# Kernel optimization log

Measured on AMD Instinct MI355X. Metric: run time of the kernel, lower is better.

Reference implementation:

```python
import jax, jax.numpy as jnp
import numpy as np

BN_EPS = 1e-5


def conv1x1(x, W, b):
    # x: [B, Cin, N], W: [Cout, Cin], b: [Cout]
    return jnp.einsum('oc,bcn->bon', W, x) + b[None, :, None]


def bn(x, p):
    # p: [4, C] rows = gamma, beta, running_mean, running_var (inference BN)
    g, be, m, v = p[0], p[1], p[2], p[3]
    inv = jax.lax.rsqrt(v + BN_EPS)
    return (x - m[None, :, None]) * (g * inv)[None, :, None] + be[None, :, None]


def conv_bn_relu(x, W, b, p):
    return jax.nn.relu(bn(conv1x1(x, W, b), p))


def _make_params(key, cout, cin):
    k1, k2 = jax.random.split(key)
    W = jax.random.normal(k1, (cout, cin), jnp.float32) * (1.0 / np.sqrt(cin))
    b = jax.random.normal(k2, (cout,), jnp.float32) * 0.01
    p = jnp.stack([jnp.ones(cout), jnp.zeros(cout), jnp.zeros(cout), jnp.ones(cout)]).astype(jnp.float32)
    return W, b, p


def setup_inputs() -> dict:
    key = jax.random.key(0)
    ks = jax.random.split(key, 16)
    B, N, S, D1, D2 = 2, 16384, 4096, 128, 256
    Cin, C, Cm = D1 + D2 + 13, 128, 128  # 397, out_channel, mlp[0]
    inp = {
        'xyz1': jax.random.normal(ks[0], (B, N, 3), jnp.float32),
        'xyz2': jax.random.normal(ks[1], (B, S, 3), jnp.float32),
        'points1': jax.random.normal(ks[2], (B, D1, N), jnp.float32),
        'points2': jax.random.normal(ks[3], (B, D2, S), jnp.float32),
        'last_pred': jax.random.normal(ks[4], (B, S, 13), jnp.float32),
    }
    inp['fuse_W'], inp['fuse_b'], inp['fuse_bn'] = _make_params(ks[5], C, Cin)
    inp['ext1_W'], inp['ext1_b'], inp['ext1_bn'] = _make_params(ks[6], C, C)
    inp['ext2_W'], inp['ext2_b'], inp['ext2_bn'] = _make_params(ks[7], C, C)
    inp['pred1_W'], inp['pred1_b'], inp['pred1_bn'] = _make_params(ks[8], Cm, C)
    inp['pred2_W'], inp['pred2_b'], inp['pred2_bn'] = _make_params(ks[9], 13, Cm)
    return inp


def _forward(xyz1, xyz2, points1, points2, last_pred,
             fuse_W, fuse_b, fuse_bn, ext1_W, ext1_b, ext1_bn,
             ext2_W, ext2_b, ext2_bn, pred1_W, pred1_b, pred1_bn,
             pred2_W, pred2_b, pred2_bn):
    B, N, _ = xyz1.shape
    p1 = jnp.transpose(points1, (0, 2, 1))  # [B, N, D1]
    p2 = jnp.transpose(points2, (0, 2, 1))  # [B, S, D2]
    # squared distances [B, N, S]
    dists = (jnp.sum(xyz1 ** 2, -1)[:, :, None]
             + jnp.sum(xyz2 ** 2, -1)[:, None, :]
             - 2.0 * jnp.einsum('bnc,bsc->bns', xyz1, xyz2))
    # 3 smallest distances (partial top-k instead of full sort; same math)
    neg_d3, idx = jax.lax.top_k(-dists, 3)  # [B, N, 3]
    d3 = -neg_d3
    recip = 1.0 / (d3 + 1e-8)
    weight = recip / jnp.sum(recip, axis=2, keepdims=True)  # [B, N, 3]
    bidx = jnp.arange(B)[:, None, None]
    interp_pts = jnp.sum(p2[bidx, idx] * weight[..., None], axis=2)        # [B, N, D2]
    interp_pred = jnp.sum(last_pred[bidx, idx] * weight[..., None], axis=2)  # [B, N, 13]
    new_points = jnp.transpose(jnp.concatenate([p1, interp_pts, interp_pred], axis=-1), (0, 2, 1))  # [B, Cin, N]
    # fuse
    x = conv_bn_relu(new_points, fuse_W, fuse_b, fuse_bn)
    # extraction: one ConvBNReLURes1D block (groups=1, res_expansion=1)
    h = conv_bn_relu(x, ext1_W, ext1_b, ext1_bn)
    x = jax.nn.relu(bn(conv1x1(h, ext2_W, ext2_b), ext2_bn) + x)  # [B, C, N]
    new_points_out = x
    # prediction head (dropout is identity in eval mode)
    feat = conv_bn_relu(x, pred1_W, pred1_b, pred1_bn)
    pred = conv_bn_relu(feat, pred2_W, pred2_b, pred2_bn)
    return (new_points_out,
            jnp.transpose(feat, (0, 2, 1)),
            jnp.transpose(pred, (0, 2, 1)))


def reference(xyz1, xyz2, points1, points2, last_pred,
              fuse_W, fuse_b, fuse_bn, ext1_W, ext1_b, ext1_bn,
              ext2_W, ext2_b, ext2_bn, pred1_W, pred1_b, pred1_bn,
              pred2_W, pred2_b, pred2_bn):
    return _forward(xyz1, xyz2, points1, points2, last_pred,
                    fuse_W, fuse_b, fuse_bn, ext1_W, ext1_b, ext1_bn,
                    ext2_W, ext2_b, ext2_bn, pred1_W, pred1_b, pred1_bn,
                    pred2_W, pred2_b, pred2_bn)
```

## Files before the change

kernel.cpp:

```cpp
#include <hip/hip_runtime.h>
#include <stdint.h>

#define B_   2
#define N_   16384
#define S_   4096
#define D2_  256
#define CIN_ 397
#define KP_  416
#define C_   128
#define OC_  13
#define NCHUNK_ 16
#define CHS_ (S_ / NCHUNK_)
#define NCAND_ (NCHUNK_ * 3)
#define XQ_P 272

typedef unsigned short u16;
typedef unsigned int u32;
typedef short s16x8 __attribute__((ext_vector_type(8)));
typedef float f32x4 __attribute__((ext_vector_type(4)));
typedef float f32x2 __attribute__((ext_vector_type(2)));

#define MFMA16(a, b, c) __builtin_amdgcn_mfma_f32_16x16x32_bf16((a), (b), (c), 0, 0, 0)

__device__ __forceinline__ float b2f(u16 h) {
  union { unsigned int u; float f; } v; v.u = ((unsigned int)h) << 16; return v.f;
}
__device__ __forceinline__ u16 f2b(float f) {
  union { float f; unsigned int u; } v; v.f = f;
  unsigned int r = v.u + 0x7fffu + ((v.u >> 16) & 1u);
  return (u16)(r >> 16);
}

#define INS3M(k0, k1, k2, key)                                            \
  do {                                                                    \
    u32 _m1, _m2;                                                         \
    asm("v_med3_u32 %0, %1, %2, %3" : "=v"(_m1) : "v"(k0), "v"(k1), "v"(key)); \
    asm("v_med3_u32 %0, %1, %2, %3" : "=v"(_m2) : "v"(k1), "v"(k2), "v"(key)); \
    k0 = min(k0, key);                                                    \
    k1 = _m1;                                                             \
    k2 = _m2;                                                             \
  } while (0)

__device__ __forceinline__ void transpose_body(
    const float* __restrict__ in, u16* __restrict__ out,
    int C, int S, int opitch, int b, int s0, int c0,
    float* __restrict__ tile, int tr, int tc4) {
  const float* ip = in + (size_t)b * C * S;
  u16* op = out + (size_t)b * S * opitch;
#pragma unroll
  for (int r = 0; r < 64; r += 16) {
    float4 v = *(const float4*)(ip + (size_t)(c0 + tr + r) * S + s0 + tc4);
    tile[(tr + r) * 65 + tc4 + 0] = v.x;
    tile[(tr + r) * 65 + tc4 + 1] = v.y;
    tile[(tr + r) * 65 + tc4 + 2] = v.z;
    tile[(tr + r) * 65 + tc4 + 3] = v.w;
  }
  __syncthreads();
#pragma unroll
  for (int r = 0; r < 64; r += 16) {
    ushort4 v;
    v.x = f2b(tile[(tc4 + 0) * 65 + tr + r]);
    v.y = f2b(tile[(tc4 + 1) * 65 + tr + r]);
    v.z = f2b(tile[(tc4 + 2) * 65 + tr + r]);
    v.w = f2b(tile[(tc4 + 3) * 65 + tr + r]);
    *(ushort4*)(op + (size_t)(s0 + tr + r) * opitch + c0 + tc4) = v;
  }
}

__global__ __launch_bounds__(256) void setup_scan_kernel(
    const float* __restrict__ xyz1, const float* __restrict__ xyz2,
    const float* __restrict__ points1, const float* __restrict__ points2,
    const float* __restrict__ fW, const float* __restrict__ fb,
    const float* __restrict__ fbn,
    const float* __restrict__ e1W, const float* __restrict__ e1b,
    const float* __restrict__ e1bn,
    const float* __restrict__ e2W, const float* __restrict__ e2b,
    const float* __restrict__ e2bn,
    const float* __restrict__ p1W, const float* __restrict__ p1b,
    const float* __restrict__ p1bn,
    const float* __restrict__ p2W, const float* __restrict__ p2b,
    const float* __restrict__ p2bn,
    u16* __restrict__ cand, u16* __restrict__ npT, u16* __restrict__ p2t,
    u16* __restrict__ Wf, u16* __restrict__ W1o,
    u16* __restrict__ W2o, u16* __restrict__ W3o,
    u16* __restrict__ Wp2, float* __restrict__ st) {
  __shared__ __align__(16) float smem[64 * 65];
  int id = blockIdx.x;
  int tid = threadIdx.x;

  if (id < 1024) {
    float* xs = smem;
    float* ys = smem + 256;
    float* zs = smem + 512;
    float* nw = smem + 768;
    int chunk = id & 15;
    int ny = (id >> 4) & 31;
    int b = id >> 9;
    int s0 = chunk * CHS_;
    const float* x2 = xyz2 + ((size_t)b * S_ + s0) * 3;
    {
      float xx = x2[tid * 3], yy = x2[tid * 3 + 1], zz = x2[tid * 3 + 2];
      xs[tid] = xx; ys[tid] = yy; zs[tid] = zz;
      nw[tid] = -0.5f * fmaf(xx, xx, fmaf(yy, yy, zz * zz));
    }
    __syncthreads();
    int nA = ny * 512 + tid;
    int nB = nA + 256;
    const float* x1a = xyz1 + ((size_t)b * N_ + nA) * 3;
    const float* x1b = xyz1 + ((size_t)b * N_ + nB) * 3;
    float axA = x1a[0], ayA = x1a[1], azA = x1a[2];
    float axB = x1b[0], ayB = x1b[1], azB = x1b[2];
    float n1A = fmaf(axA, axA, fmaf(ayA, ayA, azA * azA));
    float n1B = fmaf(axB, axB, fmaf(ayB, ayB, azB * azB));
    f32x2 axA2 = {axA, axA}, ayA2 = {ayA, ayA}, azA2 = {azA, azA};
    f32x2 axB2 = {axB, axB}, ayB2 = {ayB, ayB}, azB2 = {azB, azB};
    f32x2 n1A2 = {n1A, n1A}, n1B2 = {n1B, n1B};
    f32x2 m2 = {-2.f, -2.f}, z2 = {0.f, 0.f};
    u32 a0 = ~0u, a1 = ~0u, a2 = ~0u, b0 = ~0u, b1 = ~0u, b2 = ~0u;
    u32 c0 = ~0u, c1 = ~0u, c2 = ~0u, d0 = ~0u, d1 = ~0u, d2 = ~0u;
#pragma unroll 2
    for (int s = 0; s < CHS_; s += 2) {
      f32x2 px = *(const f32x2*)(xs + s);
      f32x2 py = *(const f32x2*)(ys + s);
      f32x2 pz = *(const f32x2*)(zs + s);
      f32x2 pw = *(const f32x2*)(nw + s);
      f32x2 dA = __builtin_elementwise_fma(azA2, pz, pw);
      dA = __builtin_elementwise_fma(ayA2, py, dA);
      dA = __builtin_elementwise_fma(axA2, px, dA);
      dA = __builtin_elementwise_fma(m2, dA, n1A2);
      dA = __builtin_elementwise_max(dA, z2);
      f32x2 dB = __builtin_elementwise_fma(azB2, pz, pw);
      dB = __builtin_elementwise_fma(ayB2, py, dB);
      dB = __builtin_elementwise_fma(axB2, px, dB);
      dB = __builtin_elementwise_fma(m2, dB, n1B2);
      dB = __builtin_elementwise_max(dB, z2);
      u32 kaA = (__float_as_uint(dA[0]) & 0xFFFFFF00u) | (u32)s;
      u32 kbA = (__float_as_uint(dA[1]) & 0xFFFFFF00u) | (u32)(s + 1);
      u32 kaB = (__float_as_uint(dB[0]) & 0xFFFFFF00u) | (u32)s;
      u32 kbB = (__float_as_uint(dB[1]) & 0xFFFFFF00u) | (u32)(s + 1);
      INS3M(a0, a1, a2, kaA);
      INS3M(b0, b1, b2, kbA);
      INS3M(c0, c1, c2, kaB);
      INS3M(d0, d1, d2, kbB);
    }
    INS3M(a0, a1, a2, b0);
    INS3M(a0, a1, a2, b1);
    INS3M(a0, a1, a2, b2);
    INS3M(c0, c1, c2, d0);
    INS3M(c0, c1, c2, d1);
    INS3M(c0, c1, c2, d2);
    u16* coA = cand + ((size_t)(b * N_ + nA)) * NCAND_ + chunk * 3;
    coA[0] = (u16)((a0 & 0xFFu) + s0);
    coA[1] = (u16)((a1 & 0xFFu) + s0);
    coA[2] = (u16)((a2 & 0xFFu) + s0);
    u16* coB = cand + ((size_t)(b * N_ + nB)) * NCAND_ + chunk * 3;
    coB[0] = (u16)((c0 & 0xFFu) + s0);
    coB[1] = (u16)((c1 & 0xFFu) + s0);
    coB[2] = (u16)((c2 & 0xFFu) + s0);
    return;
  }

  int tr = tid >> 4;
  int tc4 = (tid & 15) * 4;
  if (id < 2048) {
    int id2 = id - 1024;
    int sx = id2 & 255, sy = (id2 >> 8) & 1, b = id2 >> 9;
    transpose_body(points1, npT, 128, N_, 128, b, sx * 64, sy * 64, smem, tr, tc4);
    return;
  }
  if (id < 2560) {
    int id2 = id - 2048;
    int sx = id2 & 63, sy = (id2 >> 6) & 3, b = id2 >> 8;
    transpose_body(points2, p2t, 256, S_, 256, b, sx * 64, sy * 64, smem, tr, tc4);
    return;
  }
  int t = (id - 2560) * 256 + tid;
  int stride = 64 * 256;
  for (int i = t; i < 128 * KP_; i += stride) {
    int m = i / KP_, k = i - m * KP_;
    Wf[i] = (k < CIN_) ? f2b(fW[m * CIN_ + k]) : (u16)0;
  }
  for (int i = t; i < 128 * 128; i += stride) {
    W1o[i] = f2b(e1W[i]);
    W2o[i] = f2b(e2W[i]);
    W3o[i] = f2b(p1W[i]);
  }
  for (int i = t; i < 16 * 128; i += stride) {
    int m = i >> 7;
    Wp2[i] = (m < OC_) ? f2b(p2W[i]) : (u16)0;
  }
  for (int i = t; i < 5 * 128; i += stride) {
    int sg = i >> 7, c = i & 127;
    const float* bn; const float* bc; int Cc = 128;
    switch (sg) {
      case 0: bn = fbn;  bc = fb;  break;
      case 1: bn = e1bn; bc = e1b; break;
      case 2: bn = e2bn; bc = e2b; break;
      case 3: bn = p1bn; bc = p1b; break;
      default: bn = p2bn; bc = p2b; Cc = OC_; break;
    }
    float s = 0.f, tt = 0.f;
    if (c < Cc) {
      float g  = bn[0 * Cc + c], be = bn[1 * Cc + c];
      float mu = bn[2 * Cc + c], vv = bn[3 * Cc + c];
      float inv = 1.0f / sqrtf(vv + 1e-5f);
      s = g * inv;
      tt = (bc[c] - mu) * s + be;
    }
    st[sg * 256 + c] = s;
    st[sg * 256 + 128 + c] = tt;
  }
}

__device__ __forceinline__ void ins3(double d, int i,
                                     double& D0, double& D1, double& D2,
                                     int& I0, int& I1, int& I2) {
  if ((d < D2) || (d == D2 && i < I2)) {
    if ((d < D1) || (d == D1 && i < I1)) {
      D2 = D1; I2 = I1;
      if ((d < D0) || (d == D0 && i < I0)) { D1 = D0; I1 = I0; D0 = d; I0 = i; }
      else                                  { D1 = d; I1 = i; }
    } else { D2 = d; I2 = i; }
  }
}

__global__ __launch_bounds__(256) void interp_kernel(
    const float* __restrict__ xyz1, const float* __restrict__ xyz2,
    const u16* __restrict__ cand, const u16* __restrict__ p2t,
    const float* __restrict__ last_pred, u16* __restrict__ xq) {
  __shared__ int   iS[32][3];
  __shared__ float wS[32][3];
  int id = blockIdx.x;
  int b = id >> 9;
  int n0 = (id & 511) * 32;
  int tid = threadIdx.x;

  {
#pragma clang fp contract(off)
    int qi = tid >> 3, part = tid & 7;
    int qg = b * N_ + n0 + qi;
    const u16* ci = cand + (size_t)qg * NCAND_ + part * 6;
    const float* x2b = xyz2 + (size_t)b * S_ * 3;
    int ii[6];
#pragma unroll
    for (int j = 0; j < 6; ++j) ii[j] = ci[j];
    float pcx[6], pcy[6], pcz[6];
#pragma unroll
    for (int j = 0; j < 6; ++j) {
      const float* p = x2b + (size_t)ii[j] * 3;
      pcx[j] = p[0]; pcy[j] = p[1]; pcz[j] = p[2];
    }
    const float* x1 = xyz1 + (size_t)qg * 3;
    double ax = x1[0], ay = x1[1], az = x1[2];
    double n1 = (ax * ax + ay * ay) + az * az;
    double D0 = 1e300, D1 = 1e300, D2v = 1e300;
    int I0 = 2147483647, I1 = 2147483647, I2 = 2147483647;
#pragma unroll
    for (int j = 0; j < 6; ++j) {
      double px = pcx[j], py = pcy[j], pz = pcz[j];
      double n2 = (px * px + py * py) + pz * pz;
      double dot = (ax * px + ay * py) + az * pz;
      double d = (n1 + n2) - 2.0 * dot;
      ins3(d, ii[j], D0, D1, D2v, I0, I1, I2);
    }
#pragma unroll
    for (int r = 0; r < 3; ++r) {
      int m = 1 << r;
      double e0 = __shfl_xor(D0, m);
      double e1 = __shfl_xor(D1, m);
      double e2 = __shfl_xor(D2v, m);
      int j0 = __shfl_xor(I0, m);
      int j1 = __shfl_xor(I1, m);
      int j2 = __shfl_xor(I2, m);
      ins3(e0, j0, D0, D1, D2v, I0, I1, I2);
      ins3(e1, j1, D0, D1, D2v, I0, I1, I2);
      ins3(e2, j2, D0, D1, D2v, I0, I1, I2);
    }
    if (part == 0) {
      double r0 = 1.0 / (D0 + 1e-8);
      double r1 = 1.0 / (D1 + 1e-8);
      double r2 = 1.0 / (D2v + 1e-8);
      double sum = (r0 + r1) + r2;
      wS[qi][0] = (float)(r0 / sum);
      wS[qi][1] = (float)(r1 / sum);
      wS[qi][2] = (float)(r2 / sum);
      iS[qi][0] = I0; iS[qi][1] = I1; iS[qi][2] = I2;
    }
  }
  __syncthreads();

  int wv = tid >> 6, lane = tid & 63;
  int q = wv * 8 + (lane >> 3);
  int cg = lane & 7;
  int n = n0 + q;
  int i0 = iS[q][0], i1 = iS[q][1], i2 = iS[q][2];
  float w0 = wS[q][0], w1 = wS[q][1], w2 = wS[q][2];
  const u16* p2b = p2t + (size_t)b * S_ * D2_;
  const u16* r0p = p2b + (size_t)i0 * D2_ + cg * 32;
  const u16* r1p = p2b + (size_t)i1 * D2_ + cg * 32;
  const u16* r2p = p2b + (size_t)i2 * D2_ + cg * 32;
  u16* xrow = xq + (size_t)(b * N_ + n) * XQ_P;
#pragma unroll
  for (int j = 0; j < 8; ++j) {
    ushort4 a = *(const ushort4*)(r0p + j * 4);
    ushort4 e = *(const ushort4*)(r1p + j * 4);
    ushort4 c = *(const ushort4*)(r2p + j * 4);
    ushort4 v;
    v.x = f2b((w0 * b2f(a.x) + w1 * b2f(e.x)) + w2 * b2f(c.x));
    v.y = f2b((w0 * b2f(a.y) + w1 * b2f(e.y)) + w2 * b2f(c.y));
    v.z = f2b((w0 * b2f(a.z) + w1 * b2f(e.z)) + w2 * b2f(c.z));
    v.w = f2b((w0 * b2f(a.w) + w1 * b2f(e.w)) + w2 * b2f(c.w));
    *(ushort4*)(xrow + cg * 32 + j * 4) = v;
  }
  if (cg == 0) {
    const float* lpb = last_pred + (size_t)b * S_ * OC_;
    u16 pv[16];
#pragma unroll
    for (int c = 0; c < 16; ++c) pv[c] = 0;
#pragma unroll
    for (int c = 0; c < OC_; ++c) {
      float l0 = lpb[(size_t)i0 * OC_ + c];
      float l1 = lpb[(size_t)i1 * OC_ + c];
      float l2 = lpb[(size_t)i2 * OC_ + c];
      pv[c] = f2b((w0 * l0 + w1 * l1) + w2 * l2);
    }
#pragma unroll
    for (int c4 = 0; c4 < 4; ++c4) {
      *(ushort4*)(xrow + 256 + c4 * 4) =
          make_ushort4(pv[c4 * 4], pv[c4 * 4 + 1], pv[c4 * 4 + 2], pv[c4 * 4 + 3]);
    }
  }
}

__device__ __forceinline__ void gemm32(const u16* __restrict__ W, const u16* xb,
                                       int l15, int lq, int wv, f32x4 acc[2][2]) {
#pragma unroll
  for (int mtl = 0; mtl < 2; ++mtl) {
    acc[mtl][0] = (f32x4){0.f, 0.f, 0.f, 0.f};
    acc[mtl][1] = (f32x4){0.f, 0.f, 0.f, 0.f};
  }
#pragma unroll
  for (int ks = 0; ks < 4; ++ks) {
    int ko = ks * 32 + lq * 8;
    s16x8 b0 = *(const s16x8*)(xb + l15 * 136 + ko);
    s16x8 b1 = *(const s16x8*)(xb + (16 + l15) * 136 + ko);
#pragma unroll
    for (int mtl = 0; mtl < 2; ++mtl) {
      s16x8 a = *(const s16x8*)(W + (size_t)((wv * 2 + mtl) * 16 + l15) * 128 + ko);
      acc[mtl][0] = MFMA16(a, b0, acc[mtl][0]);
      acc[mtl][1] = MFMA16(a, b1, acc[mtl][1]);
    }
  }
}

__global__ __launch_bounds__(256, 4) void gemm_kernel(
    const u16* __restrict__ npT, const u16* __restrict__ xq,
    const u16* __restrict__ Wf,
    const u16* __restrict__ W1, const u16* __restrict__ W2,
    const u16* __restrict__ W3, const u16* __restrict__ Wp2,
    const float* __restrict__ st, float* __restrict__ out) {
  __shared__ __align__(16) u16 xb0[32 * 136];
  __shared__ __align__(16) u16 xb1[32 * 136];
  int b = blockIdx.y;
  int n0 = blockIdx.x * 32;
  int tid = threadIdx.x;
  int wv = tid >> 6, lane = tid & 63;
  int l15 = lane & 15, lq = lane >> 4;
  f32x4 acc[2][2];

#pragma unroll
  for (int mtl = 0; mtl < 2; ++mtl) {
    acc[mtl][0] = (f32x4){0.f, 0.f, 0.f, 0.f};
    acc[mtl][1] = (f32x4){0.f, 0.f, 0.f, 0.f};
  }
  {
    const u16* brow0 = npT + ((size_t)(b * N_ + n0 + l15)) * 128;
    const u16* brow1 = brow0 + (size_t)16 * 128;
#pragma unroll 2
    for (int ks = 0; ks < 4; ++ks) {
      int ko = ks * 32 + lq * 8;
      s16x8 bf0 = *(const s16x8*)(brow0 + ko);
      s16x8 bf1 = *(const s16x8*)(brow1 + ko);
#pragma unroll
      for (int mtl = 0; mtl < 2; ++mtl) {
        s16x8 a = *(const s16x8*)(Wf + (size_t)((wv * 2 + mtl) * 16 + l15) * KP_ + ko);
        acc[mtl][0] = MFMA16(a, bf0, acc[mtl][0]);
        acc[mtl][1] = MFMA16(a, bf1, acc[mtl][1]);
      }
    }
    const u16* qrow0 = xq + ((size_t)(b * N_ + n0 + l15)) * XQ_P;
    const u16* qrow1 = qrow0 + (size_t)16 * XQ_P;
#pragma unroll 3
    for (int ks = 0; ks < 9; ++ks) {
      int col = ks * 32 + lq * 8;
      s16x8 bf0 = {0, 0, 0, 0, 0, 0, 0, 0};
      s16x8 bf1 = {0, 0, 0, 0, 0, 0, 0, 0};
      if (ks < 8 || lq < 2) {
        bf0 = *(const s16x8*)(qrow0 + col);
        bf1 = *(const s16x8*)(qrow1 + col);
      }
#pragma unroll
      for (int mtl = 0; mtl < 2; ++mtl) {
        s16x8 a = *(const s16x8*)(Wf + (size_t)((wv * 2 + mtl) * 16 + l15) * KP_ + 128 + col);
        acc[mtl][0] = MFMA16(a, bf0, acc[mtl][0]);
        acc[mtl][1] = MFMA16(a, bf1, acc[mtl][1]);
      }
    }
  }
#pragma unroll
  for (int mtl = 0; mtl < 2; ++mtl) {
    int m4 = (wv * 2 + mtl) * 16 + lq * 4;
    f32x4 sc = *(const f32x4*)(st + 0 * 256 + m4);
    f32x4 bi = *(const f32x4*)(st + 0 * 256 + 128 + m4);
#pragma unroll
    for (int nt = 0; nt < 2; ++nt) {
      int n_l = nt * 16 + l15;
      ushort4 v;
      v.x = f2b(fmaxf(acc[mtl][nt][0] * sc[0] + bi[0], 0.f));
      v.y = f2b(fmaxf(acc[mtl][nt][1] * sc[1] + bi[1], 0.f));
      v.z = f2b(fmaxf(acc[mtl][nt][2] * sc[2] + bi[2], 0.f));
      v.w = f2b(fmaxf(acc[mtl][nt][3] * sc[3] + bi[3], 0.f));
      *(ushort4*)(&xb0[n_l * 136 + m4]) = v;
    }
  }
  __syncthreads();

  gemm32(W1, xb0, l15, lq, wv, acc);
#pragma unroll
  for (int mtl = 0; mtl < 2; ++mtl) {
    int m4 = (wv * 2 + mtl) * 16 + lq * 4;
    f32x4 sc = *(const f32x4*)(st + 1 * 256 + m4);
    f32x4 bi = *(const f32x4*)(st + 1 * 256 + 128 + m4);
#pragma unroll
    for (int nt = 0; nt < 2; ++nt) {
      int n_l = nt * 16 + l15;
      ushort4 v;
      v.x = f2b(fmaxf(acc[mtl][nt][0] * sc[0] + bi[0], 0.f));
      v.y = f2b(fmaxf(acc[mtl][nt][1] * sc[1] + bi[1], 0.f));
      v.z = f2b(fmaxf(acc[mtl][nt][2] * sc[2] + bi[2], 0.f));
      v.w = f2b(fmaxf(acc[mtl][nt][3] * sc[3] + bi[3], 0.f));
      *(ushort4*)(&xb1[n_l * 136 + m4]) = v;
    }
  }
  __syncthreads();

  gemm32(W2, xb1, l15, lq, wv, acc);
#pragma unroll
  for (int mtl = 0; mtl < 2; ++mtl) {
    int m4 = (wv * 2 + mtl) * 16 + lq * 4;
    f32x4 sc = *(const f32x4*)(st + 2 * 256 + m4);
    f32x4 bi = *(const f32x4*)(st + 2 * 256 + 128 + m4);
#pragma unroll
    for (int nt = 0; nt < 2; ++nt) {
      int n_l = nt * 16 + l15;
      int n_g = n0 + n_l;
      ushort4 xp = *(const ushort4*)(&xb0[n_l * 136 + m4]);
      float v0 = fmaxf(acc[mtl][nt][0] * sc[0] + bi[0] + b2f(xp.x), 0.f);
      float v1 = fmaxf(acc[mtl][nt][1] * sc[1] + bi[1] + b2f(xp.y), 0.f);
      float v2 = fmaxf(acc[mtl][nt][2] * sc[2] + bi[2] + b2f(xp.z), 0.f);
      float v3 = fmaxf(acc[mtl][nt][3] * sc[3] + bi[3] + b2f(xp.w), 0.f);
      ushort4 v;
      v.x = f2b(v0); v.y = f2b(v1); v.z = f2b(v2); v.w = f2b(v3);
      *(ushort4*)(&xb0[n_l * 136 + m4]) = v;
      out[((size_t)(b * C_ + m4 + 0)) * N_ + n_g] = v0;
      out[((size_t)(b * C_ + m4 + 1)) * N_ + n_g] = v1;
      out[((size_t)(b * C_ + m4 + 2)) * N_ + n_g] = v2;
      out[((size_t)(b * C_ + m4 + 3)) * N_ + n_g] = v3;
    }
  }
  __syncthreads();

  gemm32(W3, xb0, l15, lq, wv, acc);
  {
    float* out1 = out + (size_t)B_ * C_ * N_;
#pragma unroll
    for (int mtl = 0; mtl < 2; ++mtl) {
      int m4 = (wv * 2 + mtl) * 16 + lq * 4;
      f32x4 sc = *(const f32x4*)(st + 3 * 256 + m4);
      f32x4 bi = *(const f32x4*)(st + 3 * 256 + 128 + m4);
#pragma unroll
      for (int nt = 0; nt < 2; ++nt) {
        int n_l = nt * 16 + l15;
        int n_g = n0 + n_l;
        float v0 = fmaxf(acc[mtl][nt][0] * sc[0] + bi[0], 0.f);
        float v1 = fmaxf(acc[mtl][nt][1] * sc[1] + bi[1], 0.f);
        float v2 = fmaxf(acc[mtl][nt][2] * sc[2] + bi[2], 0.f);
        float v3 = fmaxf(acc[mtl][nt][3] * sc[3] + bi[3], 0.f);
        ushort4 v;
        v.x = f2b(v0); v.y = f2b(v1); v.z = f2b(v2); v.w = f2b(v3);
        *(ushort4*)(&xb1[n_l * 136 + m4]) = v;
        float4 o4 = make_float4(v0, v1, v2, v3);
        *(float4*)(out1 + ((size_t)(b * N_ + n_g)) * 128 + m4) = o4;
      }
    }
  }
  __syncthreads();

  if (wv < 2) {
    f32x4 a2 = (f32x4){0.f, 0.f, 0.f, 0.f};
#pragma unroll
    for (int ks = 0; ks < 4; ++ks) {
      int ko = ks * 32 + lq * 8;
      s16x8 b0 = *(const s16x8*)(&xb1[(wv * 16 + l15) * 136 + ko]);
      s16x8 a = *(const s16x8*)(Wp2 + (size_t)l15 * 128 + ko);
      a2 = MFMA16(a, b0, a2);
    }
    float* out2 = out + (size_t)B_ * C_ * N_ + (size_t)B_ * N_ * 128;
    f32x4 sc = *(const f32x4*)(st + 4 * 256 + lq * 4);
    f32x4 bi = *(const f32x4*)(st + 4 * 256 + 128 + lq * 4);
    int n_g = n0 + wv * 16 + l15;
#pragma unroll
    for (int r = 0; r < 4; ++r) {
      int m = lq * 4 + r;
      if (m < OC_) {
        out2[((size_t)(b * N_ + n_g)) * OC_ + m] =
            fmaxf(a2[r] * sc[r] + bi[r], 0.f);
      }
    }
  }
}

extern "C" void kernel_launch(void* const* d_in, const int* in_sizes, int n_in,
                              void* d_out, int out_size, void* d_ws, size_t ws_size,
                              hipStream_t stream) {
  const float* xyz1      = (const float*)d_in[0];
  const float* xyz2      = (const float*)d_in[1];
  const float* points1   = (const float*)d_in[2];
  const float* points2   = (const float*)d_in[3];
  const float* last_pred = (const float*)d_in[4];
  const float* fuse_W    = (const float*)d_in[5];
  const float* fuse_b    = (const float*)d_in[6];
  const float* fuse_bn   = (const float*)d_in[7];
  const float* ext1_W    = (const float*)d_in[8];
  const float* ext1_b    = (const float*)d_in[9];
  const float* ext1_bn   = (const float*)d_in[10];
  const float* ext2_W    = (const float*)d_in[11];
  const float* ext2_b    = (const float*)d_in[12];
  const float* ext2_bn   = (const float*)d_in[13];
  const float* pred1_W   = (const float*)d_in[14];
  const float* pred1_b   = (const float*)d_in[15];
  const float* pred1_bn  = (const float*)d_in[16];
  const float* pred2_W   = (const float*)d_in[17];
  const float* pred2_b   = (const float*)d_in[18];
  const float* pred2_bn  = (const float*)d_in[19];

  char* ws = (char*)d_ws;
  u16*   npT  = (u16*)(ws + 0);
  u16*   p2t  = (u16*)(ws + 8388608);
  u16*   cand = (u16*)(ws + 12582912);
  u16*   Wf   = (u16*)(ws + 15728640);
  u16*   W1   = (u16*)(ws + 15835136);
  u16*   W2   = (u16*)(ws + 15867904);
  u16*   W3   = (u16*)(ws + 15900672);
  u16*   Wp2  = (u16*)(ws + 15933440);
  float* st   = (float*)(ws + 15937536);
  u16*   xq   = (u16*)(ws + 15942656);

  setup_scan_kernel<<<dim3(2624), dim3(256), 0, stream>>>(
      xyz1, xyz2, points1, points2,
      fuse_W, fuse_b, fuse_bn, ext1_W, ext1_b, ext1_bn, ext2_W, ext2_b, ext2_bn,
      pred1_W, pred1_b, pred1_bn, pred2_W, pred2_b, pred2_bn,
      cand, npT, p2t, Wf, W1, W2, W3, Wp2, st);

  interp_kernel<<<dim3(1024), dim3(256), 0, stream>>>(
      xyz1, xyz2, cand, p2t, last_pred, xq);

  gemm_kernel<<<dim3(N_ / 32, B_), dim3(256), 0, stream>>>(
      npT, xq, Wf, W1, W2, W3, Wp2, st, (float*)d_out);
}
```

Baseline: 219.0 us.

## Fuse points1 transpose into GEMM and process four queries per scan thread

The separate points1 transpose into a bf16 workspace is removed. The GEMM kernel now reads fp32 points1 directly, converts it and stages it transposed in shared memory, which removes one global write and read round trip of the 8 MB intermediate. The kNN scan blocks now handle four query points per thread instead of two, halving the scan block count and reusing each shared-memory load of xyz2 across more queries. In exchange, register pressure rises in the scan, and the GEMM gains a strided shared-memory transpose store plus extra barriers.

```diff
diff --git a/kernel.cpp b/kernel.cpp
--- a/kernel.cpp
+++ b/kernel.cpp
@@ -69,7 +69,7 @@
 
 __global__ __launch_bounds__(256) void setup_scan_kernel(
     const float* __restrict__ xyz1, const float* __restrict__ xyz2,
-    const float* __restrict__ points1, const float* __restrict__ points2,
+    const float* __restrict__ points2,
     const float* __restrict__ fW, const float* __restrict__ fb,
     const float* __restrict__ fbn,
     const float* __restrict__ e1W, const float* __restrict__ e1b,
@@ -80,7 +80,7 @@
     const float* __restrict__ p1bn,
     const float* __restrict__ p2W, const float* __restrict__ p2b,
     const float* __restrict__ p2bn,
-    u16* __restrict__ cand, u16* __restrict__ npT, u16* __restrict__ p2t,
+    u16* __restrict__ cand, u16* __restrict__ p2t,
     u16* __restrict__ Wf, u16* __restrict__ W1o,
     u16* __restrict__ W2o, u16* __restrict__ W3o,
     u16* __restrict__ Wp2, float* __restrict__ st) {
@@ -88,14 +88,14 @@
   int id = blockIdx.x;
   int tid = threadIdx.x;
 
-  if (id < 1024) {
+  if (id < 512) {
     float* xs = smem;
     float* ys = smem + 256;
     float* zs = smem + 512;
     float* nw = smem + 768;
     int chunk = id & 15;
-    int ny = (id >> 4) & 31;
-    int b = id >> 9;
+    int ny = (id >> 4) & 15;
+    int b = id >> 8;
     int s0 = chunk * CHS_;
     const float* x2 = xyz2 + ((size_t)b * S_ + s0) * 3;
     {
@@ -104,77 +104,65 @@
       nw[tid] = -0.5f * fmaf(xx, xx, fmaf(yy, yy, zz * zz));
     }
     __syncthreads();
-    int nA = ny * 512 + tid;
-    int nB = nA + 256;
-    const float* x1a = xyz1 + ((size_t)b * N_ + nA) * 3;
-    const float* x1b = xyz1 + ((size_t)b * N_ + nB) * 3;
-    float axA = x1a[0], ayA = x1a[1], azA = x1a[2];
-    float axB = x1b[0], ayB = x1b[1], azB = x1b[2];
-    float n1A = fmaf(axA, axA, fmaf(ayA, ayA, azA * azA));
-    float n1B = fmaf(axB, axB, fmaf(ayB, ayB, azB * azB));
-    f32x2 axA2 = {axA, axA}, ayA2 = {ayA, ayA}, azA2 = {azA, azA};
-    f32x2 axB2 = {axB, axB}, ayB2 = {ayB, ayB}, azB2 = {azB, azB};
-    f32x2 n1A2 = {n1A, n1A}, n1B2 = {n1B, n1B};
+    int nA = ny * 1024 + tid;
+    float qx[4], qy[4], qz[4], n1[4];
+#pragma unroll
+    for (int q = 0; q < 4; ++q) {
+      const float* x1 = xyz1 + ((size_t)b * N_ + nA + q * 256) * 3;
+      qx[q] = x1[0]; qy[q] = x1[1]; qz[q] = x1[2];
+      n1[q] = fmaf(qx[q], qx[q], fmaf(qy[q], qy[q], qz[q] * qz[q]));
+    }
+    u32 K[4][2][3];
+#pragma unroll
+    for (int q = 0; q < 4; ++q)
+#pragma unroll
+      for (int e = 0; e < 2; ++e)
+#pragma unroll
+        for (int r = 0; r < 3; ++r) K[q][e][r] = ~0u;
     f32x2 m2 = {-2.f, -2.f}, z2 = {0.f, 0.f};
-    u32 a0 = ~0u, a1 = ~0u, a2 = ~0u, b0 = ~0u, b1 = ~0u, b2 = ~0u;
-    u32 c0 = ~0u, c1 = ~0u, c2 = ~0u, d0 = ~0u, d1 = ~0u, d2 = ~0u;
 #pragma unroll 2
     for (int s = 0; s < CHS_; s += 2) {
       f32x2 px = *(const f32x2*)(xs + s);
       f32x2 py = *(const f32x2*)(ys + s);
       f32x2 pz = *(const f32x2*)(zs + s);
       f32x2 pw = *(const f32x2*)(nw + s);
-      f32x2 dA = __builtin_elementwise_fma(azA2, pz, pw);
-      dA = __builtin_elementwise_fma(ayA2, py, dA);
-      dA = __builtin_elementwise_fma(axA2, px, dA);
-      dA = __builtin_elementwise_fma(m2, dA, n1A2);
-      dA = __builtin_elementwise_max(dA, z2);
-      f32x2 dB = __builtin_elementwise_fma(azB2, pz, pw);
-      dB = __builtin_elementwise_fma(ayB2, py, dB);
-      dB = __builtin_elementwise_fma(axB2, px, dB);
-      dB = __builtin_elementwise_fma(m2, dB, n1B2);
-      dB = __builtin_elementwise_max(dB, z2);
-      u32 kaA = (__float_as_uint(dA[0]) & 0xFFFFFF00u) | (u32)s;
-      u32 kbA = (__float_as_uint(dA[1]) & 0xFFFFFF00u) | (u32)(s + 1);
-      u32 kaB = (__float_as_uint(dB[0]) & 0xFFFFFF00u) | (u32)s;
-      u32 kbB = (__float_as_uint(dB[1]) & 0xFFFFFF00u) | (u32)(s + 1);
-      INS3M(a0, a1, a2, kaA);
-      INS3M(b0, b1, b2, kbA);
-      INS3M(c0, c1, c2, kaB);
-      INS3M(d0, d1, d2, kbB);
-    }
-    INS3M(a0, a1, a2, b0);
-    INS3M(a0, a1, a2, b1);
-    INS3M(a0, a1, a2, b2);
-    INS3M(c0, c1, c2, d0);
-    INS3M(c0, c1, c2, d1);
-    INS3M(c0, c1, c2, d2);
-    u16* coA = cand + ((size_t)(b * N_ + nA)) * NCAND_ + chunk * 3;
-    coA[0] = (u16)((a0 & 0xFFu) + s0);
-    coA[1] = (u16)((a1 & 0xFFu) + s0);
-    coA[2] = (u16)((a2 & 0xFFu) + s0);
-    u16* coB = cand + ((size_t)(b * N_ + nB)) * NCAND_ + chunk * 3;
-    coB[0] = (u16)((c0 & 0xFFu) + s0);
-    coB[1] = (u16)((c1 & 0xFFu) + s0);
-    coB[2] = (u16)((c2 & 0xFFu) + s0);
+#pragma unroll
+      for (int q = 0; q < 4; ++q) {
+        f32x2 ax2 = {qx[q], qx[q]}, ay2 = {qy[q], qy[q]}, az2 = {qz[q], qz[q]};
+        f32x2 n12 = {n1[q], n1[q]};
+        f32x2 d = __builtin_elementwise_fma(az2, pz, pw);
+        d = __builtin_elementwise_fma(ay2, py, d);
+        d = __builtin_elementwise_fma(ax2, px, d);
+        d = __builtin_elementwise_fma(m2, d, n12);
+        d = __builtin_elementwise_max(d, z2);
+        u32 k0 = (__float_as_uint(d[0]) & 0xFFFFFF00u) | (u32)s;
+        u32 k1 = (__float_as_uint(d[1]) & 0xFFFFFF00u) | (u32)(s + 1);
+        INS3M(K[q][0][0], K[q][0][1], K[q][0][2], k0);
+        INS3M(K[q][1][0], K[q][1][1], K[q][1][2], k1);
+      }
+    }
+#pragma unroll
+    for (int q = 0; q < 4; ++q) {
+      INS3M(K[q][0][0], K[q][0][1], K[q][0][2], K[q][1][0]);
+      INS3M(K[q][0][0], K[q][0][1], K[q][0][2], K[q][1][1]);
+      INS3M(K[q][0][0], K[q][0][1], K[q][0][2], K[q][1][2]);
+      u16* co = cand + ((size_t)(b * N_ + nA + q * 256)) * NCAND_ + chunk * 3;
+      co[0] = (u16)((K[q][0][0] & 0xFFu) + s0);
+      co[1] = (u16)((K[q][0][1] & 0xFFu) + s0);
+      co[2] = (u16)((K[q][0][2] & 0xFFu) + s0);
+    }
     return;
   }
 
   int tr = tid >> 4;
   int tc4 = (tid & 15) * 4;
-  if (id < 2048) {
-    int id2 = id - 1024;
-    int sx = id2 & 255, sy = (id2 >> 8) & 1, b = id2 >> 9;
-    transpose_body(points1, npT, 128, N_, 128, b, sx * 64, sy * 64, smem, tr, tc4);
-    return;
-  }
-  if (id < 2560) {
-    int id2 = id - 2048;
+  if (id < 1024) {
+    int id2 = id - 512;
     int sx = id2 & 63, sy = (id2 >> 6) & 3, b = id2 >> 8;
     transpose_body(points2, p2t, 256, S_, 256, b, sx * 64, sy * 64, smem, tr, tc4);
     return;
   }
-  int t = (id - 2560) * 256 + tid;
+  int t = (id - 1024) * 256 + tid;
   int stride = 64 * 256;
   for (int i = t; i < 128 * KP_; i += stride) {
     int m = i / KP_, k = i - m * KP_;
@@ -354,7 +342,7 @@
 }
 
 __global__ __launch_bounds__(256, 4) void gemm_kernel(
-    const u16* __restrict__ npT, const u16* __restrict__ xq,
+    const float* __restrict__ points1, const u16* __restrict__ xq,
     const u16* __restrict__ Wf,
     const u16* __restrict__ W1, const u16* __restrict__ W2,
     const u16* __restrict__ W3, const u16* __restrict__ Wp2,
@@ -368,19 +356,33 @@
   int l15 = lane & 15, lq = lane >> 4;
   f32x4 acc[2][2];
 
+  {
+    int n4 = (tid & 7) * 4;
+    int cb = tid >> 3;
+    const float* p1b = points1 + (size_t)b * C_ * N_;
+#pragma unroll
+    for (int rep = 0; rep < 4; ++rep) {
+      int c = cb + rep * 32;
+      float4 v = *(const float4*)(p1b + (size_t)c * N_ + n0 + n4);
+      xb1[(n4 + 0) * 136 + c] = f2b(v.x);
+      xb1[(n4 + 1) * 136 + c] = f2b(v.y);
+      xb1[(n4 + 2) * 136 + c] = f2b(v.z);
+      xb1[(n4 + 3) * 136 + c] = f2b(v.w);
+    }
+  }
+  __syncthreads();
+
 #pragma unroll
   for (int mtl = 0; mtl < 2; ++mtl) {
     acc[mtl][0] = (f32x4){0.f, 0.f, 0.f, 0.f};
     acc[mtl][1] = (f32x4){0.f, 0.f, 0.f, 0.f};
   }
   {
-    const u16* brow0 = npT + ((size_t)(b * N_ + n0 + l15)) * 128;
-    const u16* brow1 = brow0 + (size_t)16 * 128;
 #pragma unroll 2
     for (int ks = 0; ks < 4; ++ks) {
       int ko = ks * 32 + lq * 8;
-      s16x8 bf0 = *(const s16x8*)(brow0 + ko);
-      s16x8 bf1 = *(const s16x8*)(brow1 + ko);
+      s16x8 bf0 = *(const s16x8*)(&xb1[l15 * 136 + ko]);
+      s16x8 bf1 = *(const s16x8*)(&xb1[(16 + l15) * 136 + ko]);
 #pragma unroll
       for (int mtl = 0; mtl < 2; ++mtl) {
         s16x8 a = *(const s16x8*)(Wf + (size_t)((wv * 2 + mtl) * 16 + l15) * KP_ + ko);
@@ -407,6 +409,7 @@
       }
     }
   }
+  __syncthreads();
 #pragma unroll
   for (int mtl = 0; mtl < 2; ++mtl) {
     int m4 = (wv * 2 + mtl) * 16 + lq * 4;
@@ -545,26 +548,25 @@
   const float* pred2_bn  = (const float*)d_in[19];
 
   char* ws = (char*)d_ws;
-  u16*   npT  = (u16*)(ws + 0);
-  u16*   p2t  = (u16*)(ws + 8388608);
-  u16*   cand = (u16*)(ws + 12582912);
-  u16*   Wf   = (u16*)(ws + 15728640);
-  u16*   W1   = (u16*)(ws + 15835136);
-  u16*   W2   = (u16*)(ws + 15867904);
-  u16*   W3   = (u16*)(ws + 15900672);
-  u16*   Wp2  = (u16*)(ws + 15933440);
-  float* st   = (float*)(ws + 15937536);
-  u16*   xq   = (u16*)(ws + 15942656);
-
-  setup_scan_kernel<<<dim3(2624), dim3(256), 0, stream>>>(
-      xyz1, xyz2, points1, points2,
+  u16*   p2t  = (u16*)(ws + 0);
+  u16*   cand = (u16*)(ws + 4194304);
+  u16*   Wf   = (u16*)(ws + 7340032);
+  u16*   W1   = (u16*)(ws + 7446528);
+  u16*   W2   = (u16*)(ws + 7479296);
+  u16*   W3   = (u16*)(ws + 7512064);
+  u16*   Wp2  = (u16*)(ws + 7544832);
+  float* st   = (float*)(ws + 7548928);
+  u16*   xq   = (u16*)(ws + 7554048);
+
+  setup_scan_kernel<<<dim3(1088), dim3(256), 0, stream>>>(
+      xyz1, xyz2, points2,
       fuse_W, fuse_b, fuse_bn, ext1_W, ext1_b, ext1_bn, ext2_W, ext2_b, ext2_bn,
       pred1_W, pred1_b, pred1_bn, pred2_W, pred2_b, pred2_bn,
-      cand, npT, p2t, Wf, W1, W2, W3, Wp2, st);
+      cand, p2t, Wf, W1, W2, W3, Wp2, st);
 
   interp_kernel<<<dim3(1024), dim3(256), 0, stream>>>(
       xyz1, xyz2, cand, p2t, last_pred, xq);
 
   gemm_kernel<<<dim3(N_ / 32, B_), dim3(256), 0, stream>>>(
-      npT, xq, Wf, W1, W2, W3, Wp2, st, (float*)d_out);
-}
+      points1, xq, Wf, W1, W2, W3, Wp2, st, (float*)d_out);
+}
```

Measured after the change: 221.1 us. About the same (+1.0%).
